# Performance work log

Measured on AMD Instinct MI355X. Metric: run time of the kernel, lower is better.

Reference implementation:

```python
import jax, jax.numpy as jnp
import numpy as np

B, T, D_Q, D_V, ATTN, FILTERS, KSIZE = 64, 2048, 1024, 512, 128, 32, 31


def setup_inputs() -> dict:
    key = jax.random.key(0)
    ks = jax.random.split(key, 10)
    query = jax.random.normal(ks[0], (B, D_Q), dtype=jnp.float32)
    values = jax.random.normal(ks[1], (B, T, D_V), dtype=jnp.float32)
    keys = jax.random.normal(ks[2], (B, T, ATTN), dtype=jnp.float32)
    state = jax.random.uniform(ks[3], (B, T), dtype=jnp.float32)
    # learned parameters
    W_q = jax.random.normal(ks[4], (D_Q, ATTN), dtype=jnp.float32) * 0.02
    conv_kernel = jax.random.normal(ks[5], (KSIZE, 1, FILTERS), dtype=jnp.float32) * 0.1  # (W, In, Out)
    conv_bias = jnp.zeros((FILTERS,), dtype=jnp.float32)
    W_loc = jax.random.normal(ks[6], (FILTERS, ATTN), dtype=jnp.float32) * 0.1
    v_att = jax.random.normal(ks[7], (ATTN, 1), dtype=jnp.float32) * 0.1
    att_bias = jax.random.normal(ks[8], (ATTN,), dtype=jnp.float32) * 0.02
    return {"query": query, "values": values, "keys": keys, "state": state,
            "W_q": W_q, "conv_kernel": conv_kernel, "conv_bias": conv_bias,
            "W_loc": W_loc, "v_att": v_att, "att_bias": att_bias}


def reference(query, values, keys, state, W_q, conv_kernel, conv_bias, W_loc, v_att, att_bias):
    # processed_query: [B, 1, ATTN]
    pq = (query @ W_q)[:, None, :]
    # location features: Conv1D same-padding over alignments [B, T, 1] -> [B, T, FILTERS]
    loc = jax.lax.conv_general_dilated(
        state[:, :, None], conv_kernel,
        window_strides=(1,), padding='SAME',
        dimension_numbers=('NWC', 'WIO', 'NWC')) + conv_bias
    ploc = loc @ W_loc                                  # [B, T, ATTN]
    score = jnp.tanh(keys + pq + ploc + att_bias) @ v_att  # [B, T, 1]
    alignment = jax.nn.softmax(score, axis=1)           # [B, T, 1]
    attention = jnp.sum(alignment * values, axis=1)     # [B, D_V]
    alignment = jnp.squeeze(alignment, axis=2)          # [B, T]
    attention_state = alignment + state                 # cumulate=True
    return (attention, alignment, attention_state)
```

## Files before the change

kernel.cpp:

```cpp
#include <hip/hip_runtime.h>
#include <hip/hip_bf16.h>

#define B 64
#define T 2048
#define D_Q 1024
#define D_V 512
#define ATTN 128
#define FILTERS 32
#define KSIZE 31

#define PQ_OFF 0
#define CW_OFF 8192
#define PB_OFF (8192 + 3968)
#define SC_OFF (8192 + 3968 + 128)

#define AT_OFF 0
#define AL_OFF 32768
#define ST_OFF (32768 + 131072)

__device__ __forceinline__ float tanh_fast(float x) {
    float e = __expf(2.f * x);
    return 1.f - 2.f / (e + 1.f);
}

__global__ void __launch_bounds__(256)
k1_precompute(const float* __restrict__ query,
              const float* __restrict__ Wq,
              const float* __restrict__ ck,
              const float* __restrict__ cbias,
              const float* __restrict__ Wl,
              const float* __restrict__ abias,
              float* __restrict__ ws) {
    int tid = threadIdx.x;
    if (blockIdx.x < B) {
        int b = blockIdx.x;
        int q = tid & 31;
        int s = tid >> 5;
        __shared__ __align__(16) float sq[D_Q];
        __shared__ float4 red[256];
        ((float4*)sq)[tid] = ((const float4*)(query + (size_t)b * D_Q))[tid];
        __syncthreads();

        const float4* Wq4 = (const float4*)Wq;
        float4 acc = make_float4(0.f, 0.f, 0.f, 0.f);
        int dbase = s << 7;
#pragma unroll 16
        for (int i = 0; i < 128; ++i) {
            int d = dbase + i;
            float sd = sq[d];
            float4 w = Wq4[(size_t)d * 32 + q];
            acc.x += sd * w.x; acc.y += sd * w.y;
            acc.z += sd * w.z; acc.w += sd * w.w;
        }
        red[tid] = acc;
        __syncthreads();
        if (tid < 128) {
            float4 o = red[tid + 128];
            acc = red[tid];
            acc.x += o.x; acc.y += o.y; acc.z += o.z; acc.w += o.w;
            red[tid] = acc;
        }
        __syncthreads();
        if (tid < 64) {
            float4 o = red[tid + 64];
            acc = red[tid];
            acc.x += o.x; acc.y += o.y; acc.z += o.z; acc.w += o.w;
            red[tid] = acc;
        }
        __syncthreads();
        if (tid < 32) {
            float4 o = red[tid + 32];
            acc = red[tid];
            acc.x += o.x; acc.y += o.y; acc.z += o.z; acc.w += o.w;
            ((float4*)(ws + PQ_OFF))[b * 32 + tid] = acc;
        }
    } else {
        __shared__ float swl[FILTERS * ATTN];
        for (int i = tid; i < FILTERS * ATTN; i += 256) swl[i] = Wl[i];
        __syncthreads();
        if (tid < ATTN) {
            int a = tid;
            for (int k = 0; k < KSIZE; ++k) {
                float acc = 0.f;
#pragma unroll
                for (int f = 0; f < FILTERS; ++f) acc += ck[k * FILTERS + f] * swl[f * ATTN + a];
                ws[CW_OFF + k * ATTN + a] = acc;
            }
            float pb = abias[a];
#pragma unroll
            for (int f = 0; f < FILTERS; ++f) pb += cbias[f] * swl[f * ATTN + a];
            ws[PB_OFF + a] = pb;
        }
    }
}

__global__ void __launch_bounds__(256)
k2_scores(const float* __restrict__ keys,
          const float* __restrict__ state,
          const float* __restrict__ vatt,
          float* __restrict__ ws) {
    int bid = blockIdx.x;
    int b = bid >> 5;
    int t0 = (bid & 31) << 6;
    int tid = threadIdx.x;
    int a = tid & 127;
    int h = tid >> 7;

    __shared__ __align__(16) float sstate[96];
    __shared__ float sred[128];

    if (tid < 96) {
        int idx = t0 + tid - 15;
        sstate[tid] = (idx >= 0 && idx < T) ? state[b * T + idx] : 0.f;
    }

    float cw[KSIZE];
#pragma unroll
    for (int k = 0; k < KSIZE; ++k) cw[k] = ws[CW_OFF + k * ATTN + a];
    float pqa = ws[PQ_OFF + b * ATTN + a] + ws[PB_OFF + a];
    float vat = vatt[a];

    __syncthreads();

    const float* keyrow = keys + ((size_t)b * T + t0) * ATTN + a;
    const float4* sv = (const float4*)sstate;

    for (int s4 = 0; s4 < 4; ++s4) {
        int ts = h * 32 + s4 * 8;
        float kv[8];
#pragma unroll
        for (int j = 0; j < 8; ++j) kv[j] = keyrow[(size_t)(ts + j) * ATTN];
        float w[40];
#pragma unroll
        for (int q = 0; q < 10; ++q) {
            float4 v = sv[(ts >> 2) + q];
            w[4 * q + 0] = v.x; w[4 * q + 1] = v.y;
            w[4 * q + 2] = v.z; w[4 * q + 3] = v.w;
        }
        float sc[8];
#pragma unroll
        for (int j = 0; j < 8; ++j) sc[j] = 0.f;
#pragma unroll
        for (int k = 0; k < KSIZE; ++k) {
#pragma unroll
            for (int j = 0; j < 8; ++j) sc[j] += w[j + k] * cw[k];
        }
#pragma unroll
        for (int j = 0; j < 8; ++j) {
            float x = kv[j] + pqa + sc[j];
            float c = tanh_fast(x) * vat;
#pragma unroll
            for (int off = 32; off >= 1; off >>= 1) c += __shfl_xor(c, off);
            if ((tid & 63) == 0) sred[(ts + j) * 2 + (a >> 6)] = c;
        }
    }
    __syncthreads();
    if (tid < 64)
        ws[SC_OFF + b * T + t0 + tid] = sred[tid * 2] + sred[tid * 2 + 1];
}

__global__ void __launch_bounds__(256)
k3_softmax(const float* __restrict__ state,
           const float* __restrict__ ws,
           float* __restrict__ out) {
    int b = blockIdx.x;
    int tid = threadIdx.x;
    __shared__ float sm[4];
    __shared__ float ssum[4];

    float s[8];
#pragma unroll
    for (int k = 0; k < 8; ++k) s[k] = ws[SC_OFF + b * T + tid + k * 256];

    float m = s[0];
#pragma unroll
    for (int k = 1; k < 8; ++k) m = fmaxf(m, s[k]);
#pragma unroll
    for (int off = 32; off >= 1; off >>= 1) m = fmaxf(m, __shfl_xor(m, off));
    if ((tid & 63) == 0) sm[tid >> 6] = m;
    __syncthreads();
    m = fmaxf(fmaxf(sm[0], sm[1]), fmaxf(sm[2], sm[3]));

    float e[8], lsum = 0.f;
#pragma unroll
    for (int k = 0; k < 8; ++k) { e[k] = __expf(s[k] - m); lsum += e[k]; }
#pragma unroll
    for (int off = 32; off >= 1; off >>= 1) lsum += __shfl_xor(lsum, off);
    if ((tid & 63) == 0) ssum[tid >> 6] = lsum;
    __syncthreads();
    float inv = 1.f / (ssum[0] + ssum[1] + ssum[2] + ssum[3]);

#pragma unroll
    for (int k = 0; k < 8; ++k) {
        int t = tid + k * 256;
        float al = e[k] * inv;
        out[AL_OFF + b * T + t] = al;
        out[ST_OFF + b * T + t] = al + state[b * T + t];
    }
    out[AT_OFF + b * D_V + tid] = 0.f;
    out[AT_OFF + b * D_V + tid + 256] = 0.f;
}

__global__ void __launch_bounds__(256)
k4_attention(const float* __restrict__ values,
             float* __restrict__ out) {
    int bid = blockIdx.x;
    int b = bid >> 5;
    int t0 = (bid & 31) << 6;
    int tid = threadIdx.x;
    int d4 = tid & 127;
    int h = tid >> 7;

    __shared__ float sal[64];
    __shared__ float4 spart[128];

    if (tid < 64) sal[tid] = out[AL_OFF + b * T + t0 + tid];
    __syncthreads();

    const float4* V = (const float4*)values + ((size_t)b * T + t0) * (D_V / 4) + d4;
    float4 acc = make_float4(0.f, 0.f, 0.f, 0.f);
#pragma unroll 8
    for (int i = 0; i < 32; ++i) {
        int tl = h * 32 + i;
        float al = sal[tl];
        float4 v = V[(size_t)tl * (D_V / 4)];
        acc.x += al * v.x; acc.y += al * v.y;
        acc.z += al * v.z; acc.w += al * v.w;
    }
    if (h == 1) spart[d4] = acc;
    __syncthreads();
    if (h == 0) {
        float4 o = spart[d4];
        acc.x += o.x; acc.y += o.y; acc.z += o.z; acc.w += o.w;
        float* dst = out + AT_OFF + b * D_V + d4 * 4;
        atomicAdd(dst + 0, acc.x);
        atomicAdd(dst + 1, acc.y);
        atomicAdd(dst + 2, acc.z);
        atomicAdd(dst + 3, acc.w);
    }
}

extern "C" void kernel_launch(void* const* d_in, const int* in_sizes, int n_in,
                              void* d_out, int out_size, void* d_ws, size_t ws_size,
                              hipStream_t stream) {
    const float* query  = (const float*)d_in[0];
    const float* values = (const float*)d_in[1];
    const float* keys   = (const float*)d_in[2];
    const float* state  = (const float*)d_in[3];
    const float* Wq     = (const float*)d_in[4];
    const float* ck     = (const float*)d_in[5];
    const float* cbias  = (const float*)d_in[6];
    const float* Wl     = (const float*)d_in[7];
    const float* vatt   = (const float*)d_in[8];
    const float* abias  = (const float*)d_in[9];
    float* out = (float*)d_out;
    float* ws  = (float*)d_ws;

    k1_precompute<<<B + 1, 256, 0, stream>>>(query, Wq, ck, cbias, Wl, abias, ws);
    k2_scores<<<B * (T / 64), 256, 0, stream>>>(keys, state, vatt, ws);
    k3_softmax<<<B, 256, 0, stream>>>(state, ws, out);
    k4_attention<<<B * (T / 64), 256, 0, stream>>>(values, out);
}
```

Measured before the change: 437.4 us.

## Fuse score, chunk-local softmax and value reduction with split-softmax combine

Merges the score, softmax and attention kernels into one fused kernel. Each 64-step chunk computes its local max, sum of exponentials and unnormalized weighted value partial, and writes them to workspace. A small combine kernel then rescales the partials flash-decoding style and writes the alignment and state outputs. This removes one launch, the global round trip of normalized alignments, and the atomics. In exchange it adds a partial-output buffer and a serial 32-way combine per batch.

```diff
diff --git a/kernel.cpp b/kernel.cpp
--- a/kernel.cpp
+++ b/kernel.cpp
@@ -13,6 +13,8 @@
 #define CW_OFF 8192
 #define PB_OFF (8192 + 3968)
 #define SC_OFF (8192 + 3968 + 128)
+#define ML_OFF (SC_OFF + 131072)
+#define PART_OFF (ML_OFF + 4096)
 
 #define AT_OFF 0
 #define AL_OFF 32768
@@ -95,19 +97,23 @@
 }
 
 __global__ void __launch_bounds__(256)
-k2_scores(const float* __restrict__ keys,
-          const float* __restrict__ state,
-          const float* __restrict__ vatt,
-          float* __restrict__ ws) {
+k2_fused(const float* __restrict__ keys,
+         const float* __restrict__ state,
+         const float* __restrict__ values,
+         const float* __restrict__ vatt,
+         float* __restrict__ ws) {
     int bid = blockIdx.x;
     int b = bid >> 5;
-    int t0 = (bid & 31) << 6;
+    int c = bid & 31;
+    int t0 = c << 6;
     int tid = threadIdx.x;
     int a = tid & 127;
     int h = tid >> 7;
 
     __shared__ __align__(16) float sstate[96];
     __shared__ float sred[128];
+    __shared__ float sal[64];
+    __shared__ float4 spart[128];
 
     if (tid < 96) {
         int idx = t0 + tid - 15;
@@ -148,75 +154,33 @@
 #pragma unroll
         for (int j = 0; j < 8; ++j) {
             float x = kv[j] + pqa + sc[j];
-            float c = tanh_fast(x) * vat;
-#pragma unroll
-            for (int off = 32; off >= 1; off >>= 1) c += __shfl_xor(c, off);
-            if ((tid & 63) == 0) sred[(ts + j) * 2 + (a >> 6)] = c;
-        }
-    }
-    __syncthreads();
-    if (tid < 64)
-        ws[SC_OFF + b * T + t0 + tid] = sred[tid * 2] + sred[tid * 2 + 1];
-}
-
-__global__ void __launch_bounds__(256)
-k3_softmax(const float* __restrict__ state,
-           const float* __restrict__ ws,
-           float* __restrict__ out) {
-    int b = blockIdx.x;
-    int tid = threadIdx.x;
-    __shared__ float sm[4];
-    __shared__ float ssum[4];
-
-    float s[8];
-#pragma unroll
-    for (int k = 0; k < 8; ++k) s[k] = ws[SC_OFF + b * T + tid + k * 256];
-
-    float m = s[0];
-#pragma unroll
-    for (int k = 1; k < 8; ++k) m = fmaxf(m, s[k]);
-#pragma unroll
-    for (int off = 32; off >= 1; off >>= 1) m = fmaxf(m, __shfl_xor(m, off));
-    if ((tid & 63) == 0) sm[tid >> 6] = m;
-    __syncthreads();
-    m = fmaxf(fmaxf(sm[0], sm[1]), fmaxf(sm[2], sm[3]));
-
-    float e[8], lsum = 0.f;
-#pragma unroll
-    for (int k = 0; k < 8; ++k) { e[k] = __expf(s[k] - m); lsum += e[k]; }
-#pragma unroll
-    for (int off = 32; off >= 1; off >>= 1) lsum += __shfl_xor(lsum, off);
-    if ((tid & 63) == 0) ssum[tid >> 6] = lsum;
-    __syncthreads();
-    float inv = 1.f / (ssum[0] + ssum[1] + ssum[2] + ssum[3]);
-
-#pragma unroll
-    for (int k = 0; k < 8; ++k) {
-        int t = tid + k * 256;
-        float al = e[k] * inv;
-        out[AL_OFF + b * T + t] = al;
-        out[ST_OFF + b * T + t] = al + state[b * T + t];
-    }
-    out[AT_OFF + b * D_V + tid] = 0.f;
-    out[AT_OFF + b * D_V + tid + 256] = 0.f;
-}
-
-__global__ void __launch_bounds__(256)
-k4_attention(const float* __restrict__ values,
-             float* __restrict__ out) {
-    int bid = blockIdx.x;
-    int b = bid >> 5;
-    int t0 = (bid & 31) << 6;
-    int tid = threadIdx.x;
+            float cc = tanh_fast(x) * vat;
+#pragma unroll
+            for (int off = 32; off >= 1; off >>= 1) cc += __shfl_xor(cc, off);
+            if ((tid & 63) == 0) sred[(ts + j) * 2 + (a >> 6)] = cc;
+        }
+    }
+    __syncthreads();
+
+    if (tid < 64) {
+        float s = sred[tid * 2] + sred[tid * 2 + 1];
+        ws[SC_OFF + b * T + t0 + tid] = s;
+        float m = s;
+#pragma unroll
+        for (int off = 32; off >= 1; off >>= 1) m = fmaxf(m, __shfl_xor(m, off));
+        float e = __expf(s - m);
+        sal[tid] = e;
+        float l = e;
+#pragma unroll
+        for (int off = 32; off >= 1; off >>= 1) l += __shfl_xor(l, off);
+        if (tid == 0) {
+            ws[ML_OFF + (b * 32 + c) * 2 + 0] = m;
+            ws[ML_OFF + (b * 32 + c) * 2 + 1] = l;
+        }
+    }
+    __syncthreads();
+
     int d4 = tid & 127;
-    int h = tid >> 7;
-
-    __shared__ float sal[64];
-    __shared__ float4 spart[128];
-
-    if (tid < 64) sal[tid] = out[AL_OFF + b * T + t0 + tid];
-    __syncthreads();
-
     const float4* V = (const float4*)values + ((size_t)b * T + t0) * (D_V / 4) + d4;
     float4 acc = make_float4(0.f, 0.f, 0.f, 0.f);
 #pragma unroll 8
@@ -232,11 +196,53 @@
     if (h == 0) {
         float4 o = spart[d4];
         acc.x += o.x; acc.y += o.y; acc.z += o.z; acc.w += o.w;
-        float* dst = out + AT_OFF + b * D_V + d4 * 4;
-        atomicAdd(dst + 0, acc.x);
-        atomicAdd(dst + 1, acc.y);
-        atomicAdd(dst + 2, acc.z);
-        atomicAdd(dst + 3, acc.w);
+        ((float4*)(ws + PART_OFF))[(size_t)(b * 32 + c) * (D_V / 4) + d4] = acc;
+    }
+}
+
+__global__ void __launch_bounds__(256)
+k_combine(const float* __restrict__ state,
+          const float* __restrict__ ws,
+          float* __restrict__ out) {
+    int b = blockIdx.x;
+    int tid = threadIdx.x;
+    __shared__ float sw[32];
+    __shared__ float sM, sinvL;
+
+    if (tid < 32) {
+        float m = ws[ML_OFF + (b * 32 + tid) * 2 + 0];
+        float l = ws[ML_OFF + (b * 32 + tid) * 2 + 1];
+        float M = m;
+#pragma unroll
+        for (int off = 16; off >= 1; off >>= 1) M = fmaxf(M, __shfl_xor(M, off));
+        float wgt = __expf(m - M);
+        sw[tid] = wgt;
+        float L = l * wgt;
+#pragma unroll
+        for (int off = 16; off >= 1; off >>= 1) L += __shfl_xor(L, off);
+        if (tid == 0) { sM = M; sinvL = 1.f / L; }
+    }
+    __syncthreads();
+
+    float M = sM, invL = sinvL;
+
+#pragma unroll
+    for (int r = 0; r < 2; ++r) {
+        int d = tid + (r << 8);
+        float acc = 0.f;
+#pragma unroll 8
+        for (int c = 0; c < 32; ++c)
+            acc += sw[c] * ws[PART_OFF + (size_t)(b * 32 + c) * D_V + d];
+        out[AT_OFF + b * D_V + d] = acc * invL;
+    }
+
+#pragma unroll
+    for (int k = 0; k < 8; ++k) {
+        int t = tid + (k << 8);
+        float s = ws[SC_OFF + b * T + t];
+        float al = __expf(s - M) * invL;
+        out[AL_OFF + b * T + t] = al;
+        out[ST_OFF + b * T + t] = al + state[b * T + t];
     }
 }
 
@@ -257,7 +263,6 @@
     float* ws  = (float*)d_ws;
 
     k1_precompute<<<B + 1, 256, 0, stream>>>(query, Wq, ck, cbias, Wl, abias, ws);
-    k2_scores<<<B * (T / 64), 256, 0, stream>>>(keys, state, vatt, ws);
-    k3_softmax<<<B, 256, 0, stream>>>(state, ws, out);
-    k4_attention<<<B * (T / 64), 256, 0, stream>>>(values, out);
-}
+    k2_fused<<<B * (T / 64), 256, 0, stream>>>(keys, state, values, vatt, ws);
+    k_combine<<<B, 256, 0, stream>>>(state, ws, out);
+}
```

Result: no change. 433.1 us (-1.0%).
